# Performance work log

Measured on AMD Instinct MI355X. Metric: run time of the kernel, lower is better.

Reference implementation:

```python
import jax, jax.numpy as jnp
import numpy as np

M = 8      # number of modalities (len(ModalityType))
D = 256    # embedding_dim
B = 8192   # batch size


def setup_inputs() -> dict:
    key = jax.random.key(0)
    ks = jax.random.split(key, 12)
    s = 1.0 / np.sqrt(D)
    x = jax.random.normal(ks[0], (M, B, D), dtype=jnp.float32)
    reasoning_query = jax.random.normal(ks[1], (B, D), dtype=jnp.float32)
    # Per ordered modality pair (src, tgt): seq_len=1 MHA reduces to out_proj(V_proj(tgt)).
    Wv = jax.random.normal(ks[2], (M, M, D, D), dtype=jnp.float32) * s
    bv = jnp.zeros((M, M, D), dtype=jnp.float32)
    Wo = jax.random.normal(ks[3], (M, M, D, D), dtype=jnp.float32) * s
    bo = jnp.zeros((M, M, D), dtype=jnp.float32)
    # Per-modality fusion MLP: Linear(2D->D), ReLU, Linear(D->D)  (dropout = eval/identity)
    W1 = jax.random.normal(ks[4], (M, D, 2 * D), dtype=jnp.float32) * s
    b1 = jnp.zeros((M, D), dtype=jnp.float32)
    W2 = jax.random.normal(ks[5], (M, D, D), dtype=jnp.float32) * s
    b2 = jnp.zeros((M, D), dtype=jnp.float32)
    # Attention controller: Linear(2D->D), ReLU, Linear(D->1), Sigmoid
    Wc1 = jax.random.normal(ks[6], (D, 2 * D), dtype=jnp.float32) * s
    bc1 = jnp.zeros((D,), dtype=jnp.float32)
    wc2 = jax.random.normal(ks[7], (D,), dtype=jnp.float32) * s
    bc2 = jnp.zeros((1,), dtype=jnp.float32)
    return dict(x=x, reasoning_query=reasoning_query, Wv=Wv, bv=bv, Wo=Wo, bo=bo,
                W1=W1, b1=b1, W2=W2, b2=b2, Wc1=Wc1, bc1=bc1, wc2=wc2, bc2=bc2)


def reference(x, reasoning_query, Wv, bv, Wo, bo, W1, b1, W2, b2, Wc1, bc1, wc2, bc2):
    m = x.shape[0]
    # Cross-modal attention with seq_len=1: softmax over one key == 1, so the
    # attended output is exactly out_proj(V_proj(tgt_embedding)) for every pair.
    h = jnp.einsum('tbd,sted->stbe', x, Wv) + bv[:, :, None, :]          # [M,M,B,D]
    ctx = jnp.einsum('stbe,stoe->stbo', h, Wo) + bo[:, :, None, :]       # [M,M,B,D]
    # Mean over the M-1 target modalities (src != tgt), matching stack(...).mean(-1)
    offdiag = (1.0 - jnp.eye(m, dtype=x.dtype))[:, :, None, None]
    cross = (ctx * offdiag).sum(axis=1) / (m - 1)                         # [M,B,D]
    # Per-modality fusion MLP on cat([original, cross])
    comb = jnp.concatenate([x, cross], axis=-1)                           # [M,B,2D]
    hid = jax.nn.relu(jnp.einsum('mbf,mdf->mbd', comb, W1) + b1[:, None, :])
    fused = jnp.einsum('mbd,mod->mbo', hid, W2) + b2[:, None, :]          # [M,B,D]
    # Reasoning-query gating controller
    q = jnp.broadcast_to(reasoning_query[None], fused.shape)              # [M,B,D]
    qc = jnp.concatenate([q, fused], axis=-1)                             # [M,B,2D]
    ch = jax.nn.relu(jnp.einsum('mbf,df->mbd', qc, Wc1) + bc1)
    score = jax.nn.sigmoid(jnp.einsum('mbd,d->mb', ch, wc2) + bc2)        # [M,B]
    gated = fused * score[..., None]
    unified = gated.mean(axis=0)                                          # [B,D]
    return unified
```

## Files before the change

### kernel.cpp

```cpp
#include <hip/hip_runtime.h>

#define MMOD 8
#define BB 8192
#define DD 256

typedef unsigned short u16;
typedef __attribute__((ext_vector_type(8))) short s16x8;
typedef __attribute__((ext_vector_type(4))) float f32x4;
typedef __attribute__((ext_vector_type(8))) unsigned short u16x8;

typedef __attribute__((address_space(3))) unsigned short lds_u16;
typedef __attribute__((address_space(1))) const unsigned short gl_u16;

__device__ __forceinline__ float b2f(u16 u){ union{unsigned i; float f;} x; x.i=((unsigned)u)<<16; return x.f; }
__device__ __forceinline__ u16 f2b(float f){ union{float f; unsigned i;} x; x.f=f; unsigned r = x.i + 0x7FFF + ((x.i>>16)&1u); return (u16)(r>>16); }

__device__ __forceinline__ void async_cp16(const u16* g, u16* l){
  __builtin_amdgcn_global_load_lds((gl_u16*)g, (lds_u16*)l, 16, 0, 0);
}

struct ConvArgs {
  const float* src[10];
  u16*         dst[10];
  int          n[10];
};
__global__ void convert_kernel(ConvArgs a){
  const long long stride = (long long)gridDim.x * blockDim.x;
  const long long base   = (long long)blockIdx.x * blockDim.x + threadIdx.x;
  for (int s = 0; s < 10; s++){
    const int n  = a.n[s];
    const int n8 = n >> 3;
    const float* sp = a.src[s];
    u16* dst = a.dst[s];
    for (long long i = base; i < n8; i += stride){
      float4 lo = ((const float4*)sp)[i*2];
      float4 hi = ((const float4*)sp)[i*2+1];
      u16x8 p;
      p[0]=f2b(lo.x); p[1]=f2b(lo.y); p[2]=f2b(lo.z); p[3]=f2b(lo.w);
      p[4]=f2b(hi.x); p[5]=f2b(hi.y); p[6]=f2b(hi.z); p[7]=f2b(hi.w);
      *(u16x8*)(dst + (i<<3)) = p;
    }
    for (long long i = ((long long)n8<<3) + base; i < n; i += stride)
      dst[i] = f2b(sp[i]);
  }
}

__device__ __forceinline__ s16x8 load8_f32(const float* p, long long idx){
  float4 lo = *(const float4*)(p + idx);
  float4 hi = *(const float4*)(p + idx + 4);
  s16x8 r;
  r[0]=(short)f2b(lo.x); r[1]=(short)f2b(lo.y); r[2]=(short)f2b(lo.z); r[3]=(short)f2b(lo.w);
  r[4]=(short)f2b(hi.x); r[5]=(short)f2b(hi.y); r[6]=(short)f2b(hi.z); r[7]=(short)f2b(hi.w);
  return r;
}

struct GArgs {
  const u16* A;  long long a_z; long long a_piece; int lda;
  const u16* A2; long long a2_z;
  const u16* B;  long long b_z; int ldb;
  u16*       C;  long long c_z; long long c_npiece; int ldc;
  const u16* bias; long long bias_z;
  const float* cbias;
  const u16* addm;
  float scale;
  int K;
  int relu;
};

__global__ __launch_bounds__(256, 2) void gemm_bt(GArgs g){
  alignas(16) __shared__ u16 lA[128*64];
  alignas(16) __shared__ u16 lB[128*64];
  const int tid  = threadIdx.x;
  const int lane = tid & 63;
  const int w    = tid >> 6;
  const int z    = blockIdx.z;

  const u16* Bbase = g.B + (long long)z * g.b_z + (long long)(blockIdx.y * 128) * g.ldb;

  f32x4 acc[4][4];
  #pragma unroll
  for (int i=0;i<4;i++)
    #pragma unroll
    for (int j=0;j<4;j++)
      #pragma unroll
      for (int r=0;r<4;r++) acc[i][j][r] = 0.0f;

  const int wr = (w >> 1) * 64, wc = (w & 1) * 64;
  const int fm = lane & 15;
  const int fk = (lane >> 4) * 8;
  const long long arow0 = (long long)blockIdx.x * 128;

  const int sr = lane >> 3;
  const int sq = (lane & 7) ^ sr;

  for (int k0 = 0; k0 < g.K; k0 += 64){
    const u16* Abase0 = (g.A2 && k0 >= 256) ? (g.A2 + (long long)z * g.a2_z)
                                            : (g.A  + (long long)z * g.a_z);
    const u16* At = Abase0 + (long long)(k0 >> 8) * g.a_piece + (k0 & 255);
    const u16* Bt = Bbase + k0;
    __syncthreads();
    #pragma unroll
    for (int i=0;i<4;i++){
      int r = i*32 + w*8 + sr;
      async_cp16(At + (arow0 + r) * (long long)g.lda + sq*8, lA + (i*256 + w*64) * 8);
      async_cp16(Bt + (long long)r * g.ldb + sq*8, lB + (i*256 + w*64) * 8);
    }
    __syncthreads();
    #pragma unroll
    for (int kk = 0; kk < 64; kk += 32){
      s16x8 af[4], bfr[4];
      const int qf = (kk + fk) >> 3;
      #pragma unroll
      for (int mi=0; mi<4; mi++){
        int r = wr + mi*16 + fm;
        af[mi] = *(const s16x8*)(lA + (r*8 + (qf ^ (r & 7))) * 8);
      }
      #pragma unroll
      for (int ni=0; ni<4; ni++){
        int r = wc + ni*16 + fm;
        bfr[ni] = *(const s16x8*)(lB + (r*8 + (qf ^ (r & 7))) * 8);
      }
      #pragma unroll
      for (int mi=0; mi<4; mi++)
        #pragma unroll
        for (int ni=0; ni<4; ni++)
          acc[mi][ni] = __builtin_amdgcn_mfma_f32_16x16x32_bf16(af[mi], bfr[ni], acc[mi][ni], 0, 0, 0);
    }
  }

  u16* Cb = g.C + (long long)z * g.c_z;
  const u16* biasp = g.bias ? g.bias + (long long)z * g.bias_z : (const u16*)0;
  #pragma unroll
  for (int mi=0; mi<4; mi++){
    #pragma unroll
    for (int ni=0; ni<4; ni++){
      int n = blockIdx.y*128 + wc + ni*16 + fm;
      float bb = 0.0f;
      if (g.cbias) bb = g.cbias[n];
      else if (biasp) bb = b2f(biasp[n]);
      long long cn = ((long long)(n >> 8)) * g.c_npiece + (n & 255);
      #pragma unroll
      for (int r=0; r<4; r++){
        long long b = arow0 + wr + mi*16 + (lane>>4)*4 + r;
        float v = acc[mi][ni][r] * g.scale + bb;
        if (g.addm) v += b2f(g.addm[b*256 + n]);
        if (g.relu) v = v > 0.0f ? v : 0.0f;
        Cb[cn + b * (long long)g.ldc] = f2b(v);
      }
    }
  }
}

__global__ __launch_bounds__(256, 4) void gemm_thin(GArgs g){
  alignas(16) __shared__ u16 lA[64*64];
  alignas(16) __shared__ u16 lB[128*64];
  const int tid  = threadIdx.x;
  const int lane = tid & 63;
  const int w    = tid >> 6;
  const int z    = blockIdx.z;

  const u16* Bbase = g.B + (long long)z * g.b_z + (long long)(blockIdx.y * 128) * g.ldb;

  f32x4 acc[8];
  #pragma unroll
  for (int j=0;j<8;j++)
    #pragma unroll
    for (int r=0;r<4;r++) acc[j][r] = 0.0f;

  const int fm = lane & 15;
  const int fk = (lane >> 4) * 8;
  const long long arow0 = (long long)blockIdx.x * 64;

  const int sr = lane >> 3;
  const int sq = (lane & 7) ^ sr;

  for (int k0 = 0; k0 < g.K; k0 += 64){
    const u16* Abase0 = (g.A2 && k0 >= 256) ? (g.A2 + (long long)z * g.a2_z)
                                            : (g.A  + (long long)z * g.a_z);
    const u16* At = Abase0 + (long long)(k0 >> 8) * g.a_piece + (k0 & 255);
    const u16* Bt = Bbase + k0;
    __syncthreads();
    #pragma unroll
    for (int i=0;i<2;i++){
      int r = i*32 + w*8 + sr;
      async_cp16(At + (arow0 + r) * (long long)g.lda + sq*8, lA + (i*256 + w*64) * 8);
    }
    #pragma unroll
    for (int i=0;i<4;i++){
      int r = i*32 + w*8 + sr;
      async_cp16(Bt + (long long)r * g.ldb + sq*8, lB + (i*256 + w*64) * 8);
    }
    __syncthreads();
    #pragma unroll
    for (int kk = 0; kk < 64; kk += 32){
      const int qf = (kk + fk) >> 3;
      int ra = w*16 + fm;
      s16x8 af = *(const s16x8*)(lA + (ra*8 + (qf ^ (ra & 7))) * 8);
      s16x8 bfr[8];
      #pragma unroll
      for (int ni=0; ni<8; ni++){
        int r = ni*16 + fm;
        bfr[ni] = *(const s16x8*)(lB + (r*8 + (qf ^ (r & 7))) * 8);
      }
      #pragma unroll
      for (int ni=0; ni<8; ni++)
        acc[ni] = __builtin_amdgcn_mfma_f32_16x16x32_bf16(af, bfr[ni], acc[ni], 0, 0, 0);
    }
  }

  u16* Cb = g.C + (long long)z * g.c_z;
  const u16* biasp = g.bias ? g.bias + (long long)z * g.bias_z : (const u16*)0;
  #pragma unroll
  for (int ni=0; ni<8; ni++){
    int n = blockIdx.y*128 + ni*16 + fm;
    float bb = 0.0f;
    if (g.cbias) bb = g.cbias[n];
    else if (biasp) bb = b2f(biasp[n]);
    long long cn = ((long long)(n >> 8)) * g.c_npiece + (n & 255);
    #pragma unroll
    for (int r=0; r<4; r++){
      long long b = arow0 + w*16 + (lane>>4)*4 + r;
      float v = acc[ni][r] * g.scale + bb;
      if (g.addm) v += b2f(g.addm[b*256 + n]);
      if (g.relu) v = v > 0.0f ? v : 0.0f;
      Cb[cn + b * (long long)g.ldc] = f2b(v);
    }
  }
}

__global__ __launch_bounds__(256, 2) void build_wb(const float* Wo, const float* Wv, u16* WB){
  alignas(16) __shared__ u16 lA[128*64];
  alignas(16) __shared__ u16 lB[128*64];
  const int tid  = threadIdx.x;
  const int lane = tid & 63;
  const int w    = tid >> 6;
  const int z = blockIdx.z, s = z >> 3, t = z & 7;
  const long long zoff = (long long)z * 65536;

  f32x4 acc[4][4];
  #pragma unroll
  for (int i=0;i<4;i++)
    #pragma unroll
    for (int j=0;j<4;j++)
      #pragma unroll
      for (int r=0;r<4;r++) acc[i][j][r] = 0.0f;

  const int wr = (w >> 1) * 64, wc = (w & 1) * 64;
  const int fm = lane & 15;
  const int fk = (lane >> 4) * 8;

  int srow[4], sq[4];
  #pragma unroll
  for (int i=0;i<4;i++){
    int c = i*256 + tid;
    srow[i] = c >> 3;
    sq[i]   = (c & 7) ^ (srow[i] & 7);
  }

  for (int k0 = 0; k0 < 256; k0 += 64){
    s16x8 va[4], vt[4];
    #pragma unroll
    for (int i=0;i<4;i++){
      long long aidx = zoff + (long long)(blockIdx.x*128 + srow[i]) * 256 + k0 + sq[i]*8;
      va[i] = load8_f32(Wo, aidx);
    }
    #pragma unroll
    for (int j=0;j<4;j++){
      int id = j*256 + tid;
      int e  = id >> 4;
      int dc = (id & 15) * 8;
      long long bidx = zoff + (long long)(k0 + e) * 256 + blockIdx.y*128 + dc;
      vt[j] = load8_f32(Wv, bidx);
    }
    __syncthreads();
    #pragma unroll
    for (int i=0;i<4;i++){
      int c = i*256 + tid;
      *(s16x8*)(lA + c*8) = va[i];
    }
    #pragma unroll
    for (int j=0;j<4;j++){
      int id = j*256 + tid;
      int e  = id >> 4;
      int dc = (id & 15) * 8;
      #pragma unroll
      for (int u=0; u<8; u++){
        int d = dc + u;
        lB[(d*8 + ((e>>3) ^ (d & 7)))*8 + (e & 7)] = (u16)vt[j][u];
      }
    }
    __syncthreads();
    #pragma unroll
    for (int kk = 0; kk < 64; kk += 32){
      s16x8 af[4], bfr[4];
      const int qf = (kk + fk) >> 3;
      #pragma unroll
      for (int mi=0; mi<4; mi++){
        int r = wr + mi*16 + fm;
        af[mi] = *(const s16x8*)(lA + (r*8 + (qf ^ (r & 7))) * 8);
      }
      #pragma unroll
      for (int ni=0; ni<4; ni++){
        int r = wc + ni*16 + fm;
        bfr[ni] = *(const s16x8*)(lB + (r*8 + (qf ^ (r & 7))) * 8);
      }
      #pragma unroll
      for (int mi=0; mi<4; mi++)
        #pragma unroll
        for (int ni=0; ni<4; ni++)
          acc[mi][ni] = __builtin_amdgcn_mfma_f32_16x16x32_bf16(af[mi], bfr[ni], acc[mi][ni], 0, 0, 0);
    }
    __syncthreads();
  }
  const int diag = (s == t);
  #pragma unroll
  for (int mi=0; mi<4; mi++){
    #pragma unroll
    for (int ni=0; ni<4; ni++){
      int d = blockIdx.y*128 + wc + ni*16 + fm;
      #pragma unroll
      for (int r=0; r<4; r++){
        int o = blockIdx.x*128 + wr + mi*16 + (lane>>4)*4 + r;
        float v = diag ? 0.0f : acc[mi][ni][r];
        WB[(long long)(s*256 + o) * 2048 + t*256 + d] = f2b(v);
      }
    }
  }
}

__global__ void cb_kernel(const float* bv, const float* Wo, const float* bo, float* cb){
  int z = blockIdx.x, s = z >> 3, t = z & 7;
  if (s == t) return;
  int o = threadIdx.x;
  long long wbase  = (long long)z * 65536 + (long long)o * 256;
  long long bvbase = (long long)z * 256;
  float acc = 0.0f;
  for (int e = 0; e < 256; e += 4){
    float4 wv4 = *(const float4*)(Wo + wbase + e);
    float4 bv4 = *(const float4*)(bv + bvbase + e);
    acc += wv4.x*bv4.x + wv4.y*bv4.y + wv4.z*bv4.z + wv4.w*bv4.w;
  }
  acc += bo[(long long)z*256 + o];
  atomicAdd(&cb[s*256 + o], acc * (1.0f/7.0f));
}

__global__ __launch_bounds__(256) void final_gate(const u16* ch, const u16* fused,
                                                  const u16* wc2b, const u16* bc2b, float* out){
  __shared__ float scores[8];
  int b = blockIdx.x;
  int tid = threadIdx.x, lane = tid & 63, w = tid >> 6;
  float bc2f = b2f(bc2b[0]);
  float wv[4];
  #pragma unroll
  for (int j=0;j<4;j++) wv[j] = b2f(wc2b[lane + 64*j]);
  #pragma unroll
  for (int half=0; half<2; half++){
    int m = w + half*4;
    const u16* cp = ch + ((long long)m*BB + b)*256;
    float p = 0.0f;
    #pragma unroll
    for (int j=0;j<4;j++) p += b2f(cp[lane + 64*j]) * wv[j];
    #pragma unroll
    for (int off=32; off>0; off>>=1) p += __shfl_down(p, off);
    if (lane == 0) scores[m] = 1.0f / (1.0f + __expf(-(p + bc2f)));
  }
  __syncthreads();
  float acc = 0.0f;
  #pragma unroll
  for (int m=0; m<8; m++)
    acc += b2f(fused[((long long)m*BB + b)*256 + tid]) * scores[m];
  out[(long long)b*256 + tid] = acc * 0.125f;
}

extern "C" void kernel_launch(void* const* d_in, const int* in_sizes, int n_in,
                              void* d_out, int out_size, void* d_ws, size_t ws_size,
                              hipStream_t stream){
  const float* x   = (const float*)d_in[0];
  const float* q   = (const float*)d_in[1];
  const float* Wv  = (const float*)d_in[2];
  const float* bv  = (const float*)d_in[3];
  const float* Wo  = (const float*)d_in[4];
  const float* bo  = (const float*)d_in[5];
  const float* W1  = (const float*)d_in[6];
  const float* b1  = (const float*)d_in[7];
  const float* W2  = (const float*)d_in[8];
  const float* b2  = (const float*)d_in[9];
  const float* Wc1 = (const float*)d_in[10];
  const float* bc1 = (const float*)d_in[11];
  const float* wc2 = (const float*)d_in[12];
  const float* bc2 = (const float*)d_in[13];

  char* ws = (char*)d_ws;
  u16*   xb    = (u16*)(ws + 0LL);
  u16*   qb    = (u16*)(ws + 33554432LL);
  u16*   cross = (u16*)(ws + 37748736LL);
  u16*   hid   = (u16*)(ws + 71303168LL);
  u16*   WB    = (u16*)(ws + 104857600LL);
  u16*   W1b   = (u16*)(ws + 113246208LL);
  u16*   W2b   = (u16*)(ws + 115343360LL);
  u16*   Wc1b  = (u16*)(ws + 116391936LL);
  u16*   b1b   = (u16*)(ws + 116654080LL);
  u16*   b2b   = (u16*)(ws + 116658176LL);
  u16*   bc1b  = (u16*)(ws + 116662272LL);
  u16*   wc2b  = (u16*)(ws + 116662784LL);
  u16*   bc2b  = (u16*)(ws + 116663296LL);
  float* cb    = (float*)(ws + 116663424LL);
  u16*   fused = xb;
  u16*   ch    = cross;
  u16*   qctx  = WB;

  ConvArgs ca{};
  ca.src[0]=x;   ca.dst[0]=xb;   ca.n[0]=MMOD*BB*DD;
  ca.src[1]=q;   ca.dst[1]=qb;   ca.n[1]=BB*DD;
  ca.src[2]=W1;  ca.dst[2]=W1b;  ca.n[2]=MMOD*DD*2*DD;
  ca.src[3]=W2;  ca.dst[3]=W2b;  ca.n[3]=MMOD*DD*DD;
  ca.src[4]=Wc1; ca.dst[4]=Wc1b; ca.n[4]=DD*2*DD;
  ca.src[5]=b1;  ca.dst[5]=b1b;  ca.n[5]=MMOD*DD;
  ca.src[6]=b2;  ca.dst[6]=b2b;  ca.n[6]=MMOD*DD;
  ca.src[7]=bc1; ca.dst[7]=bc1b; ca.n[7]=DD;
  ca.src[8]=wc2; ca.dst[8]=wc2b; ca.n[8]=DD;
  ca.src[9]=bc2; ca.dst[9]=bc2b; ca.n[9]=1;
  convert_kernel<<<1024, 256, 0, stream>>>(ca);

  hipMemsetAsync(cb, 0, 2048*sizeof(float), stream);
  build_wb<<<dim3(2,2,64), 256, 0, stream>>>(Wo, Wv, WB);
  cb_kernel<<<dim3(64), 256, 0, stream>>>(bv, Wo, bo, cb);

  const long long BD = (long long)BB * DD;

  GArgs g2{};
  g2.A = xb; g2.a_z = 0; g2.a_piece = BD; g2.lda = 256; g2.A2 = 0; g2.a2_z = 0;
  g2.B = WB; g2.b_z = 0; g2.ldb = 2048;
  g2.C = cross; g2.c_z = 0; g2.c_npiece = BD; g2.ldc = 256;
  g2.bias = 0; g2.bias_z = 0; g2.cbias = cb; g2.addm = 0;
  g2.scale = 1.0f/7.0f; g2.K = 2048; g2.relu = 0;
  gemm_bt<<<dim3(64,16,1), 256, 0, stream>>>(g2);

  GArgs g5a{};
  g5a.A = qb; g5a.a_z = 0; g5a.a_piece = 0; g5a.lda = 256; g5a.A2 = 0; g5a.a2_z = 0;
  g5a.B = Wc1b; g5a.b_z = 0; g5a.ldb = 512;
  g5a.C = qctx; g5a.c_z = 0; g5a.c_npiece = 0; g5a.ldc = 256;
  g5a.bias = 0; g5a.bias_z = 0; g5a.cbias = 0; g5a.addm = 0;
  g5a.scale = 1.0f; g5a.K = 256; g5a.relu = 0;
  gemm_thin<<<dim3(128,2,1), 256, 0, stream>>>(g5a);

  GArgs g3{};
  g3.A = xb; g3.a_z = BD; g3.a_piece = 0; g3.lda = 256; g3.A2 = cross; g3.a2_z = BD;
  g3.B = W1b; g3.b_z = (long long)DD*2*DD; g3.ldb = 512;
  g3.C = hid; g3.c_z = BD; g3.c_npiece = 0; g3.ldc = 256;
  g3.bias = b1b; g3.bias_z = 256; g3.cbias = 0; g3.addm = 0;
  g3.scale = 1.0f; g3.K = 512; g3.relu = 1;
  gemm_thin<<<dim3(128,2,8), 256, 0, stream>>>(g3);

  GArgs g4{};
  g4.A = hid; g4.a_z = BD; g4.a_piece = 0; g4.lda = 256; g4.A2 = 0; g4.a2_z = 0;
  g4.B = W2b; g4.b_z = (long long)DD*DD; g4.ldb = 256;
  g4.C = fused; g4.c_z = BD; g4.c_npiece = 0; g4.ldc = 256;
  g4.bias = b2b; g4.bias_z = 256; g4.cbias = 0; g4.addm = 0;
  g4.scale = 1.0f; g4.K = 256; g4.relu = 0;
  gemm_thin<<<dim3(128,2,8), 256, 0, stream>>>(g4);

  GArgs g5b{};
  g5b.A = fused; g5b.a_z = BD; g5b.a_piece = 0; g5b.lda = 256; g5b.A2 = 0; g5b.a2_z = 0;
  g5b.B = Wc1b + 256; g5b.b_z = 0; g5b.ldb = 512;
  g5b.C = ch; g5b.c_z = BD; g5b.c_npiece = 0; g5b.ldc = 256;
  g5b.bias = bc1b; g5b.bias_z = 0; g5b.cbias = 0; g5b.addm = qctx;
  g5b.scale = 1.0f; g5b.K = 256; g5b.relu = 1;
  gemm_thin<<<dim3(128,2,8), 256, 0, stream>>>(g5b);

  final_gate<<<dim3(BB), 256, 0, stream>>>(ch, fused, wc2b, bc2b, (float*)d_out);

  (void)in_sizes; (void)n_in; (void)out_size; (void)ws_size;
}
```

Measured before the change: 374.0 us.

## Fuse controller score into GEMM epilogue and widen thin GEMM tiles to full N

Adds a gemm_score kernel that computes the controller hidden layer, applies ReLU, dots it with wc2 and applies the sigmoid inside the epilogue. It writes only per-row scores, so the [M,B,D] ch tensor is never stored or reread by final_gate. gemm_thin now covers all 256 output columns per block, so each A tile is loaded once instead of twice, at the cost of more accumulators and twice the B LDS. cb_kernel is also reworked into coalesced row-wise reductions with more blocks, and bc2 is copied as fp32.

```diff
diff --git a/kernel.cpp b/kernel.cpp
--- a/kernel.cpp
+++ b/kernel.cpp
@@ -62,6 +62,8 @@
   const u16* bias; long long bias_z;
   const float* cbias;
   const u16* addm;
+  const u16* wc2;
+  float*     scores;
   float scale;
   int K;
   int relu;
@@ -153,17 +155,17 @@
 
 __global__ __launch_bounds__(256, 4) void gemm_thin(GArgs g){
   alignas(16) __shared__ u16 lA[64*64];
-  alignas(16) __shared__ u16 lB[128*64];
+  alignas(16) __shared__ u16 lB[256*64];
   const int tid  = threadIdx.x;
   const int lane = tid & 63;
   const int w    = tid >> 6;
   const int z    = blockIdx.z;
 
-  const u16* Bbase = g.B + (long long)z * g.b_z + (long long)(blockIdx.y * 128) * g.ldb;
-
-  f32x4 acc[8];
-  #pragma unroll
-  for (int j=0;j<8;j++)
+  const u16* Bbase = g.B + (long long)z * g.b_z;
+
+  f32x4 acc[16];
+  #pragma unroll
+  for (int j=0;j<16;j++)
     #pragma unroll
     for (int r=0;r<4;r++) acc[j][r] = 0.0f;
 
@@ -186,7 +188,7 @@
       async_cp16(At + (arow0 + r) * (long long)g.lda + sq*8, lA + (i*256 + w*64) * 8);
     }
     #pragma unroll
-    for (int i=0;i<4;i++){
+    for (int i=0;i<8;i++){
       int r = i*32 + w*8 + sr;
       async_cp16(Bt + (long long)r * g.ldb + sq*8, lB + (i*256 + w*64) * 8);
     }
@@ -196,34 +198,111 @@
       const int qf = (kk + fk) >> 3;
       int ra = w*16 + fm;
       s16x8 af = *(const s16x8*)(lA + (ra*8 + (qf ^ (ra & 7))) * 8);
-      s16x8 bfr[8];
-      #pragma unroll
-      for (int ni=0; ni<8; ni++){
+      #pragma unroll
+      for (int ni=0; ni<16; ni++){
         int r = ni*16 + fm;
-        bfr[ni] = *(const s16x8*)(lB + (r*8 + (qf ^ (r & 7))) * 8);
-      }
-      #pragma unroll
-      for (int ni=0; ni<8; ni++)
-        acc[ni] = __builtin_amdgcn_mfma_f32_16x16x32_bf16(af, bfr[ni], acc[ni], 0, 0, 0);
+        s16x8 bfr = *(const s16x8*)(lB + (r*8 + (qf ^ (r & 7))) * 8);
+        acc[ni] = __builtin_amdgcn_mfma_f32_16x16x32_bf16(af, bfr, acc[ni], 0, 0, 0);
+      }
     }
   }
 
   u16* Cb = g.C + (long long)z * g.c_z;
   const u16* biasp = g.bias ? g.bias + (long long)z * g.bias_z : (const u16*)0;
   #pragma unroll
-  for (int ni=0; ni<8; ni++){
-    int n = blockIdx.y*128 + ni*16 + fm;
+  for (int ni=0; ni<16; ni++){
+    int n = ni*16 + fm;
     float bb = 0.0f;
     if (g.cbias) bb = g.cbias[n];
     else if (biasp) bb = b2f(biasp[n]);
-    long long cn = ((long long)(n >> 8)) * g.c_npiece + (n & 255);
     #pragma unroll
     for (int r=0; r<4; r++){
       long long b = arow0 + w*16 + (lane>>4)*4 + r;
       float v = acc[ni][r] * g.scale + bb;
       if (g.addm) v += b2f(g.addm[b*256 + n]);
       if (g.relu) v = v > 0.0f ? v : 0.0f;
-      Cb[cn + b * (long long)g.ldc] = f2b(v);
+      Cb[b * (long long)g.ldc + n] = f2b(v);
+    }
+  }
+}
+
+__global__ __launch_bounds__(256, 4) void gemm_score(GArgs g){
+  alignas(16) __shared__ u16 lA[64*64];
+  alignas(16) __shared__ u16 lB[256*64];
+  const int tid  = threadIdx.x;
+  const int lane = tid & 63;
+  const int w    = tid >> 6;
+  const int z    = blockIdx.z;
+
+  const u16* Bbase = g.B;
+
+  f32x4 acc[16];
+  #pragma unroll
+  for (int j=0;j<16;j++)
+    #pragma unroll
+    for (int r=0;r<4;r++) acc[j][r] = 0.0f;
+
+  const int fm = lane & 15;
+  const int fk = (lane >> 4) * 8;
+  const long long arow0 = (long long)blockIdx.x * 64;
+
+  const int sr = lane >> 3;
+  const int sq = (lane & 7) ^ sr;
+
+  for (int k0 = 0; k0 < g.K; k0 += 64){
+    const u16* At = g.A + (long long)z * g.a_z + k0;
+    const u16* Bt = Bbase + k0;
+    __syncthreads();
+    #pragma unroll
+    for (int i=0;i<2;i++){
+      int r = i*32 + w*8 + sr;
+      async_cp16(At + (arow0 + r) * (long long)g.lda + sq*8, lA + (i*256 + w*64) * 8);
+    }
+    #pragma unroll
+    for (int i=0;i<8;i++){
+      int r = i*32 + w*8 + sr;
+      async_cp16(Bt + (long long)r * g.ldb + sq*8, lB + (i*256 + w*64) * 8);
+    }
+    __syncthreads();
+    #pragma unroll
+    for (int kk = 0; kk < 64; kk += 32){
+      const int qf = (kk + fk) >> 3;
+      int ra = w*16 + fm;
+      s16x8 af = *(const s16x8*)(lA + (ra*8 + (qf ^ (ra & 7))) * 8);
+      #pragma unroll
+      for (int ni=0; ni<16; ni++){
+        int r = ni*16 + fm;
+        s16x8 bfr = *(const s16x8*)(lB + (r*8 + (qf ^ (r & 7))) * 8);
+        acc[ni] = __builtin_amdgcn_mfma_f32_16x16x32_bf16(af, bfr, acc[ni], 0, 0, 0);
+      }
+    }
+  }
+
+  float p[4] = {0.f, 0.f, 0.f, 0.f};
+  #pragma unroll
+  for (int ni=0; ni<16; ni++){
+    int n = ni*16 + fm;
+    float bb = b2f(g.bias[n]);
+    float wcv = b2f(g.wc2[n]);
+    #pragma unroll
+    for (int r=0; r<4; r++){
+      long long b = arow0 + w*16 + (lane>>4)*4 + r;
+      float v = acc[ni][r] + bb + b2f(g.addm[b*256 + n]);
+      v = v > 0.0f ? v : 0.0f;
+      p[r] += v * wcv;
+    }
+  }
+  #pragma unroll
+  for (int r=0; r<4; r++){
+    #pragma unroll
+    for (int off=1; off<16; off<<=1) p[r] += __shfl_xor(p[r], off);
+  }
+  if (fm == 0){
+    float bc2f = g.cbias[0];
+    #pragma unroll
+    for (int r=0; r<4; r++){
+      long long b = arow0 + w*16 + (lane>>4)*4 + r;
+      g.scores[(long long)z*BB + b] = 1.0f / (1.0f + __expf(-(p[r] + bc2f)));
     }
   }
 }
@@ -328,47 +407,33 @@
   }
 }
 
-__global__ void cb_kernel(const float* bv, const float* Wo, const float* bo, float* cb){
+__global__ __launch_bounds__(256) void cb_kernel(const float* bv, const float* Wo, const float* bo, float* cb){
   int z = blockIdx.x, s = z >> 3, t = z & 7;
   if (s == t) return;
-  int o = threadIdx.x;
-  long long wbase  = (long long)z * 65536 + (long long)o * 256;
-  long long bvbase = (long long)z * 256;
+  int lane = threadIdx.x & 63, w = threadIdx.x >> 6;
+  float4 bvv = *(const float4*)(bv + (long long)z*256 + lane*4);
+  #pragma unroll
+  for (int i=0; i<16; i++){
+    int row = blockIdx.y*64 + w*16 + i;
+    float4 wv4 = *(const float4*)(Wo + (long long)z*65536 + (long long)row*256 + lane*4);
+    float p = wv4.x*bvv.x + wv4.y*bvv.y + wv4.z*bvv.z + wv4.w*bvv.w;
+    #pragma unroll
+    for (int off=32; off>0; off>>=1) p += __shfl_xor(p, off);
+    if (lane == 0)
+      atomicAdd(&cb[s*256 + row], (p + bo[(long long)z*256 + row]) * (1.0f/7.0f));
+  }
+}
+
+__global__ __launch_bounds__(256) void final_gate(const u16* fused, const float* scores, float* out){
+  int b = blockIdx.x;
+  int tid = threadIdx.x;
+  float sc[8];
+  #pragma unroll
+  for (int m=0; m<8; m++) sc[m] = scores[(long long)m*BB + b];
   float acc = 0.0f;
-  for (int e = 0; e < 256; e += 4){
-    float4 wv4 = *(const float4*)(Wo + wbase + e);
-    float4 bv4 = *(const float4*)(bv + bvbase + e);
-    acc += wv4.x*bv4.x + wv4.y*bv4.y + wv4.z*bv4.z + wv4.w*bv4.w;
-  }
-  acc += bo[(long long)z*256 + o];
-  atomicAdd(&cb[s*256 + o], acc * (1.0f/7.0f));
-}
-
-__global__ __launch_bounds__(256) void final_gate(const u16* ch, const u16* fused,
-                                                  const u16* wc2b, const u16* bc2b, float* out){
-  __shared__ float scores[8];
-  int b = blockIdx.x;
-  int tid = threadIdx.x, lane = tid & 63, w = tid >> 6;
-  float bc2f = b2f(bc2b[0]);
-  float wv[4];
-  #pragma unroll
-  for (int j=0;j<4;j++) wv[j] = b2f(wc2b[lane + 64*j]);
-  #pragma unroll
-  for (int half=0; half<2; half++){
-    int m = w + half*4;
-    const u16* cp = ch + ((long long)m*BB + b)*256;
-    float p = 0.0f;
-    #pragma unroll
-    for (int j=0;j<4;j++) p += b2f(cp[lane + 64*j]) * wv[j];
-    #pragma unroll
-    for (int off=32; off>0; off>>=1) p += __shfl_down(p, off);
-    if (lane == 0) scores[m] = 1.0f / (1.0f + __expf(-(p + bc2f)));
-  }
-  __syncthreads();
-  float acc = 0.0f;
   #pragma unroll
   for (int m=0; m<8; m++)
-    acc += b2f(fused[((long long)m*BB + b)*256 + tid]) * scores[m];
+    acc += b2f(fused[((long long)m*BB + b)*256 + tid]) * sc[m];
   out[(long long)b*256 + tid] = acc * 0.125f;
 }
 
@@ -403,11 +468,11 @@
   u16*   b2b   = (u16*)(ws + 116658176LL);
   u16*   bc1b  = (u16*)(ws + 116662272LL);
   u16*   wc2b  = (u16*)(ws + 116662784LL);
-  u16*   bc2b  = (u16*)(ws + 116663296LL);
+  float* bc2f  = (float*)(ws + 116663296LL);
   float* cb    = (float*)(ws + 116663424LL);
   u16*   fused = xb;
-  u16*   ch    = cross;
   u16*   qctx  = WB;
+  float* scores = (float*)(ws + 104857600LL + 4194304LL);
 
   ConvArgs ca{};
   ca.src[0]=x;   ca.dst[0]=xb;   ca.n[0]=MMOD*BB*DD;
@@ -419,12 +484,13 @@
   ca.src[6]=b2;  ca.dst[6]=b2b;  ca.n[6]=MMOD*DD;
   ca.src[7]=bc1; ca.dst[7]=bc1b; ca.n[7]=DD;
   ca.src[8]=wc2; ca.dst[8]=wc2b; ca.n[8]=DD;
-  ca.src[9]=bc2; ca.dst[9]=bc2b; ca.n[9]=1;
+  ca.src[9]=bc2; ca.dst[9]=bc1b; ca.n[9]=0;
   convert_kernel<<<1024, 256, 0, stream>>>(ca);
+  hipMemcpyAsync(bc2f, bc2, sizeof(float), hipMemcpyDeviceToDevice, stream);
 
   hipMemsetAsync(cb, 0, 2048*sizeof(float), stream);
   build_wb<<<dim3(2,2,64), 256, 0, stream>>>(Wo, Wv, WB);
-  cb_kernel<<<dim3(64), 256, 0, stream>>>(bv, Wo, bo, cb);
+  cb_kernel<<<dim3(64,4), 256, 0, stream>>>(bv, Wo, bo, cb);
 
   const long long BD = (long long)BB * DD;
 
@@ -432,7 +498,7 @@
   g2.A = xb; g2.a_z = 0; g2.a_piece = BD; g2.lda = 256; g2.A2 = 0; g2.a2_z = 0;
   g2.B = WB; g2.b_z = 0; g2.ldb = 2048;
   g2.C = cross; g2.c_z = 0; g2.c_npiece = BD; g2.ldc = 256;
-  g2.bias = 0; g2.bias_z = 0; g2.cbias = cb; g2.addm = 0;
+  g2.bias = 0; g2.bias_z = 0; g2.cbias = cb; g2.addm = 0; g2.wc2 = 0; g2.scores = 0;
   g2.scale = 1.0f/7.0f; g2.K = 2048; g2.relu = 0;
   gemm_bt<<<dim3(64,16,1), 256, 0, stream>>>(g2);
 
@@ -440,35 +506,36 @@
   g5a.A = qb; g5a.a_z = 0; g5a.a_piece = 0; g5a.lda = 256; g5a.A2 = 0; g5a.a2_z = 0;
   g5a.B = Wc1b; g5a.b_z = 0; g5a.ldb = 512;
   g5a.C = qctx; g5a.c_z = 0; g5a.c_npiece = 0; g5a.ldc = 256;
-  g5a.bias = 0; g5a.bias_z = 0; g5a.cbias = 0; g5a.addm = 0;
+  g5a.bias = 0; g5a.bias_z = 0; g5a.cbias = 0; g5a.addm = 0; g5a.wc2 = 0; g5a.scores = 0;
   g5a.scale = 1.0f; g5a.K = 256; g5a.relu = 0;
-  gemm_thin<<<dim3(128,2,1), 256, 0, stream>>>(g5a);
+  gemm_thin<<<dim3(128,1,1), 256, 0, stream>>>(g5a);
 
   GArgs g3{};
   g3.A = xb; g3.a_z = BD; g3.a_piece = 0; g3.lda = 256; g3.A2 = cross; g3.a2_z = BD;
   g3.B = W1b; g3.b_z = (long long)DD*2*DD; g3.ldb = 512;
   g3.C = hid; g3.c_z = BD; g3.c_npiece = 0; g3.ldc = 256;
-  g3.bias = b1b; g3.bias_z = 256; g3.cbias = 0; g3.addm = 0;
+  g3.bias = b1b; g3.bias_z = 256; g3.cbias = 0; g3.addm = 0; g3.wc2 = 0; g3.scores = 0;
   g3.scale = 1.0f; g3.K = 512; g3.relu = 1;
-  gemm_thin<<<dim3(128,2,8), 256, 0, stream>>>(g3);
+  gemm_thin<<<dim3(128,1,8), 256, 0, stream>>>(g3);
 
   GArgs g4{};
   g4.A = hid; g4.a_z = BD; g4.a_piece = 0; g4.lda = 256; g4.A2 = 0; g4.a2_z = 0;
   g4.B = W2b; g4.b_z = (long long)DD*DD; g4.ldb = 256;
   g4.C = fused; g4.c_z = BD; g4.c_npiece = 0; g4.ldc = 256;
-  g4.bias = b2b; g4.bias_z = 256; g4.cbias = 0; g4.addm = 0;
+  g4.bias = b2b; g4.bias_z = 256; g4.cbias = 0; g4.addm = 0; g4.wc2 = 0; g4.scores = 0;
   g4.scale = 1.0f; g4.K = 256; g4.relu = 0;
-  gemm_thin<<<dim3(128,2,8), 256, 0, stream>>>(g4);
+  gemm_thin<<<dim3(128,1,8), 256, 0, stream>>>(g4);
 
   GArgs g5b{};
   g5b.A = fused; g5b.a_z = BD; g5b.a_piece = 0; g5b.lda = 256; g5b.A2 = 0; g5b.a2_z = 0;
   g5b.B = Wc1b + 256; g5b.b_z = 0; g5b.ldb = 512;
-  g5b.C = ch; g5b.c_z = BD; g5b.c_npiece = 0; g5b.ldc = 256;
-  g5b.bias = bc1b; g5b.bias_z = 0; g5b.cbias = 0; g5b.addm = qctx;
+  g5b.C = 0; g5b.c_z = 0; g5b.c_npiece = 0; g5b.ldc = 0;
+  g5b.bias = bc1b; g5b.bias_z = 0; g5b.cbias = bc2f; g5b.addm = qctx;
+  g5b.wc2 = wc2b; g5b.scores = scores;
   g5b.scale = 1.0f; g5b.K = 256; g5b.relu = 1;
-  gemm_thin<<<dim3(128,2,8), 256, 0, stream>>>(g5b);
-
-  final_gate<<<dim3(BB), 256, 0, stream>>>(ch, fused, wc2b, bc2b, (float*)d_out);
+  gemm_score<<<dim3(128,1,8), 256, 0, stream>>>(g5b);
+
+  final_gate<<<dim3(BB), 256, 0, stream>>>(fused, scores, (float*)d_out);
 
   (void)in_sizes; (void)n_in; (void)out_size; (void)ws_size;
 }
```

Result: faster. 349.0 us (-6.7%).
